# Optimization experiments

Hardware: AMD Instinct MI355X
Metric: run time of the kernel (lower is better)

Reference implementation:

```python
import jax, jax.numpy as jnp
import numpy as np

N, P, K, H, W = 16, 2048, 512, 256, 256
ZTHRESH = 2.0          # PRUN_ZSCORE_THRESHOLD
MULT = 5               # HV_HYPOTHESIS_IN_MASK_MULTIPLIER


def setup_inputs() -> dict:
    key = jax.random.key(0)
    uv_img = jax.random.normal(key, (N, 2, H, W), dtype=jnp.float32)
    rng = np.random.default_rng(0)
    # mask points per instance (torch.where(mask[i]) made fixed-shape)
    pts = rng.integers(0, H, size=(N, P, 2)).astype(np.int32)
    # multinomial pair sampling without replacement: distinct indices per pair
    i0 = rng.integers(0, P, size=(N, K))
    off = rng.integers(1, P, size=(N, K))
    i1 = (i0 + off) % P
    pair_idx = np.stack([i0, i1], axis=-1).astype(np.int32)
    return {"uv_img": uv_img, "pts": jnp.asarray(pts), "pair_idx": jnp.asarray(pair_idx)}


def _gather_uv(uv_img, coords):
    # uv_img: [N,2,H,W], coords: [N,M,2] int -> [N,M,2] uv values
    n, _, h, w = uv_img.shape
    flat = coords[..., 0] * w + coords[..., 1]            # [N,M]
    uv_flat = uv_img.reshape(n, 2, h * w)                 # [N,2,HW]
    g = jnp.take_along_axis(uv_flat, flat[:, None, :], axis=2)  # [N,2,M]
    return jnp.transpose(g, (0, 2, 1))                    # [N,M,2]


def reference(uv_img, pts, pair_idx):
    # --- generate hypotheses (batched pinverse solver) ---
    p0 = jnp.take_along_axis(pts, pair_idx[..., 0:1], axis=1)  # [N,K,2]
    p1 = jnp.take_along_axis(pts, pair_idx[..., 1:2], axis=1)  # [N,K,2]
    uv0 = _gather_uv(uv_img, p0)                               # [N,K,2]
    uv1 = _gather_uv(uv_img, p1)                               # [N,K,2]
    A = jnp.stack((uv0, -uv1), axis=-1)                        # [N,K,2,2]
    Bv = (p1 - p0).astype(jnp.float32)[..., None]              # [N,K,2,1]  (-p0 + p1)
    X = jnp.matmul(jnp.linalg.pinv(A), Bv)                     # [N,K,2,1]
    x0 = X[:, :, 0, :]                                         # [N,K,1]
    Y = x0 * uv0 + p0.astype(jnp.float32)                      # [N,K,2] hypotheses

    # --- prune outliers (z-score, drop -> nan in torch; here masked) ---
    mean = jnp.mean(Y, axis=1, keepdims=True)
    std = jnp.std(Y, axis=1, keepdims=True, ddof=1)
    z = jnp.abs((Y - mean) / std)
    bad = jnp.any(z > ZTHRESH, axis=-1) | jnp.any(jnp.isnan(Y), axis=-1)  # [N,K]
    Yz = jnp.where(bad[..., None], 0.0, Y)                     # nan-hypotheses zeroed (as torch does)

    # --- hypothesis weights ---
    ptsf = pts.astype(jnp.float32)                             # [N,P,2]
    uv_p = _gather_uv(uv_img, pts)                             # [N,P,2]
    d = Y[:, :, None, :] - ptsf[:, None, :, :]                 # [N,K,P,2]
    a = d / jnp.linalg.norm(d, axis=-1, keepdims=True)
    b = jnp.einsum('nkpc,npc->nkp', a, uv_p) > 0               # direction agreement
    w = jnp.sum(b, axis=-1)                                    # [N,K] int
    match = Y.astype(jnp.int32)[:, :, None, :] == pts[:, None, :, :]
    h_in_mask = jnp.sum(match[..., 0] & match[..., 1], axis=-1)  # [N,K]
    factor = jnp.where(h_in_mask == 1, MULT, 1)
    w = (factor * w).astype(jnp.float32)
    w = jnp.where(bad, 0.0, w)                                 # outlier rows get 0 weight
    w = w / jnp.maximum(jnp.sum(w, axis=1, keepdims=True), 1.0)

    weighted_mean = jnp.sum(Yz * w[..., None], axis=1)         # [N,2]
    pixel_xy = weighted_mean[:, ::-1]                          # (row,col) -> (x,y)
    return pixel_xy
```

## Files before the change

kernel.cpp:

```cpp
#include <hip/hip_runtime.h>
#include <math.h>

#define N_ 16
#define P_ 2048
#define K_ 512
#define H_ 256
#define W_ 256
#define HW_ (H_ * W_)
#define ZT_ 2.0f
#define GBLK_ 128
#define KB_ 32
#define KPB_ 16

__global__ __launch_bounds__(256) void k_pre(
    const float* __restrict__ uv_img, const int* __restrict__ pts,
    const int* __restrict__ pair, float2* __restrict__ uvp,
    float2* __restrict__ Yg, int* __restrict__ bad, int* __restrict__ done) {
  int tid = threadIdx.x;
  if (blockIdx.x < GBLK_) {
    int id = blockIdx.x * 256 + tid;
    int2 c = ((const int2*)pts)[id];
    const float* base = uv_img + (size_t)(id >> 11) * 2 * HW_;
    int o = c.x * W_ + c.y;
    uvp[id] = make_float2(base[o], base[HW_ + o]);
    return;
  }
  int n = blockIdx.x - GBLK_;
  if (tid == 0) done[n] = 0;
  const int2* pts2 = (const int2*)pts + n * P_;
  const int2* pr2 = (const int2*)pair + n * K_;
  const float* base = uv_img + (size_t)n * 2 * HW_;

  float2 ya, yb;
#pragma unroll
  for (int h = 0; h < 2; h++) {
    int k = tid + h * 256;
    int2 pr = pr2[k];
    int2 p0 = pts2[pr.x];
    int2 p1 = pts2[pr.y];
    float u00 = base[p0.x * W_ + p0.y];
    float u01 = base[HW_ + p0.x * W_ + p0.y];
    float u10 = base[p1.x * W_ + p1.y];
    float u11 = base[HW_ + p1.x * W_ + p1.y];
    float B0 = (float)(p1.x - p0.x);
    float B1 = (float)(p1.y - p0.y);
    float det = u10 * u01 - u00 * u11;
    float x0 = (u10 * B1 - B0 * u11) / det;
    float2 y = make_float2(x0 * u00 + (float)p0.x, x0 * u01 + (float)p0.y);
    if (h == 0) ya = y; else yb = y;
    Yg[n * K_ + k] = y;
  }

  __shared__ float red[4][2];
  __shared__ float bc[4];
  int wave = tid >> 6, lane = tid & 63;
  float a0 = ya.x + yb.x, a1 = ya.y + yb.y;
  for (int off = 32; off >= 1; off >>= 1) {
    a0 += __shfl_down(a0, off);
    a1 += __shfl_down(a1, off);
  }
  if (lane == 0) { red[wave][0] = a0; red[wave][1] = a1; }
  __syncthreads();
  if (tid == 0) {
    float t0 = red[0][0] + red[1][0] + red[2][0] + red[3][0];
    float t1 = red[0][1] + red[1][1] + red[2][1] + red[3][1];
    bc[0] = t0 / (float)K_;
    bc[1] = t1 / (float)K_;
  }
  __syncthreads();
  float m0 = bc[0], m1 = bc[1];
  float ea0 = ya.x - m0, ea1 = ya.y - m1;
  float eb0 = yb.x - m0, eb1 = yb.y - m1;
  a0 = ea0 * ea0 + eb0 * eb0;
  a1 = ea1 * ea1 + eb1 * eb1;
  for (int off = 32; off >= 1; off >>= 1) {
    a0 += __shfl_down(a0, off);
    a1 += __shfl_down(a1, off);
  }
  if (lane == 0) { red[wave][0] = a0; red[wave][1] = a1; }
  __syncthreads();
  if (tid == 0) {
    float t0 = red[0][0] + red[1][0] + red[2][0] + red[3][0];
    float t1 = red[0][1] + red[1][1] + red[2][1] + red[3][1];
    bc[2] = sqrtf(t0 / (float)(K_ - 1));
    bc[3] = sqrtf(t1 / (float)(K_ - 1));
  }
  __syncthreads();
  float sd0 = bc[2], sd1 = bc[3];
  int bda = (fabsf(ea0 / sd0) > ZT_) | (fabsf(ea1 / sd1) > ZT_) |
            (ya.x != ya.x) | (ya.y != ya.y);
  int bdb = (fabsf(eb0 / sd0) > ZT_) | (fabsf(eb1 / sd1) > ZT_) |
            (yb.x != yb.x) | (yb.y != yb.y);
  bad[n * K_ + tid] = bda;
  bad[n * K_ + tid + 256] = bdb;
}

__global__ __launch_bounds__(256) void k_vote(
    const int* __restrict__ pts, const float2* __restrict__ uvp,
    const float2* __restrict__ Yg, const int* __restrict__ bad,
    float* __restrict__ pw, float* __restrict__ ps0, float* __restrict__ ps1,
    int* __restrict__ done, float* __restrict__ out) {
  int b = blockIdx.x, tid = threadIdx.x;
  int n = b >> 5, kt = b & (KB_ - 1);
  __shared__ float4 sf[P_];
  __shared__ float red[4][3];
  __shared__ int sflag;
  const int2* pts2 = (const int2*)pts + n * P_;
  const float2* uvn = uvp + n * P_;

#pragma unroll
  for (int j = 0; j < 8; j++) {
    int p = j * 256 + tid;
    int2 pc = pts2[p];
    float2 uc = uvn[p];
    float c = (float)pc.x * uc.x + (float)pc.y * uc.y;
    int pk = (pc.x << 8) | pc.y;
    sf[p] = make_float4(uc.x, uc.y, c, __int_as_float(pk));
  }

  int k = kt * KPB_ + (tid >> 4);
  int pl = tid & 15;
  float2 yk = Yg[n * K_ + k];
  int iy0 = (int)yk.x, iy1 = (int)yk.y;
  int mk = (((unsigned)iy0 < 256u) & ((unsigned)iy1 < 256u))
               ? ((iy0 << 8) | iy1) : -1;
  __syncthreads();

  int cnt = 0, hm = 0;
#pragma unroll 8
  for (int i = 0; i < P_ / 16; i++) {
    float4 f = sf[pl + (i << 4)];
    float dot = fmaf(yk.x, f.x, fmaf(yk.y, f.y, -f.z));
    cnt += (dot > 0.f) ? 1 : 0;
    hm += (__float_as_int(f.w) == mk) ? 1 : 0;
  }

  for (int off = 8; off >= 1; off >>= 1) {
    cnt += __shfl_down(cnt, off, 16);
    hm += __shfl_down(hm, off, 16);
  }
  float w = 0.f, s0 = 0.f, s1 = 0.f;
  if (pl == 0 && !bad[n * K_ + k]) {
    w = (float)cnt * ((hm == 1) ? 5.0f : 1.0f);
    s0 = w * yk.x;
    s1 = w * yk.y;
  }
  for (int off = 32; off >= 1; off >>= 1) {
    w += __shfl_down(w, off);
    s0 += __shfl_down(s0, off);
    s1 += __shfl_down(s1, off);
  }
  int wave = tid >> 6, lane = tid & 63;
  if (lane == 0) { red[wave][0] = w; red[wave][1] = s0; red[wave][2] = s1; }
  __syncthreads();
  if (tid == 0) {
    float tw = red[0][0] + red[1][0] + red[2][0] + red[3][0];
    float t0 = red[0][1] + red[1][1] + red[2][1] + red[3][1];
    float t1 = red[0][2] + red[1][2] + red[2][2] + red[3][2];
    pw[b] = tw;
    ps0[b] = t0;
    ps1[b] = t1;
    int old = __hip_atomic_fetch_add(&done[n], 1, __ATOMIC_ACQ_REL,
                                     __HIP_MEMORY_SCOPE_AGENT);
    sflag = (old == KB_ - 1);
  }
  __syncthreads();
  if (sflag && tid < KB_) {
    int i = (n << 5) + tid;
    float fw = __hip_atomic_load(&pw[i], __ATOMIC_RELAXED,
                                 __HIP_MEMORY_SCOPE_AGENT);
    float f0 = __hip_atomic_load(&ps0[i], __ATOMIC_RELAXED,
                                 __HIP_MEMORY_SCOPE_AGENT);
    float f1 = __hip_atomic_load(&ps1[i], __ATOMIC_RELAXED,
                                 __HIP_MEMORY_SCOPE_AGENT);
    for (int off = 16; off >= 1; off >>= 1) {
      fw += __shfl_down(fw, off, 32);
      f0 += __shfl_down(f0, off, 32);
      f1 += __shfl_down(f1, off, 32);
    }
    if (tid == 0) {
      float den = fmaxf(fw, 1.0f);
      out[n * 2 + 0] = f1 / den;
      out[n * 2 + 1] = f0 / den;
    }
  }
}

extern "C" void kernel_launch(void* const* d_in, const int* in_sizes, int n_in,
                              void* d_out, int out_size, void* d_ws,
                              size_t ws_size, hipStream_t stream) {
  const float* uv_img = (const float*)d_in[0];
  const int* pts = (const int*)d_in[1];
  const int* pair = (const int*)d_in[2];
  float* out = (float*)d_out;

  float2* uvp = (float2*)d_ws;
  float2* Yg = uvp + N_ * P_;
  int* bad = (int*)(Yg + N_ * K_);
  float* pw = (float*)(bad + N_ * K_);
  float* ps0 = pw + N_ * KB_;
  float* ps1 = ps0 + N_ * KB_;
  int* done = (int*)(ps1 + N_ * KB_);

  hipLaunchKernelGGL(k_pre, dim3(GBLK_ + N_), dim3(256), 0, stream, uv_img,
                     pts, pair, uvp, Yg, bad, done);
  hipLaunchKernelGGL(k_vote, dim3(N_ * KB_), dim3(256), 0, stream, pts, uvp,
                     Yg, bad, pw, ps0, ps1, done, out);
}
```

Measured before the change: 26.46 us.

## Register-tile hypotheses per thread and stream points directly, dropping shared staging

After: 27.35 us. 1.03x slower.

```diff
diff --git a/kernel.cpp b/kernel.cpp
--- a/kernel.cpp
+++ b/kernel.cpp
@@ -102,64 +102,77 @@
     int* __restrict__ done, float* __restrict__ out) {
   int b = blockIdx.x, tid = threadIdx.x;
   int n = b >> 5, kt = b & (KB_ - 1);
-  __shared__ float4 sf[P_];
+  int wave = tid >> 6, lane = tid & 63;
+  __shared__ unsigned redc[4][KPB_];
   __shared__ float red[4][3];
   __shared__ int sflag;
+
+  float ykx[KPB_], yky[KPB_];
+  int mk[KPB_];
+#pragma unroll
+  for (int j = 0; j < KPB_; j++) {
+    float2 y = Yg[n * K_ + kt * KPB_ + j];
+    ykx[j] = y.x;
+    yky[j] = y.y;
+    int iy0 = (int)y.x, iy1 = (int)y.y;
+    mk[j] = (((unsigned)iy0 < 256u) & ((unsigned)iy1 < 256u))
+                ? ((iy0 << 8) | iy1) : -1;
+  }
+
   const int2* pts2 = (const int2*)pts + n * P_;
   const float2* uvn = uvp + n * P_;
-
-#pragma unroll
-  for (int j = 0; j < 8; j++) {
-    int p = j * 256 + tid;
+  unsigned acc[KPB_];
+#pragma unroll
+  for (int j = 0; j < KPB_; j++) acc[j] = 0u;
+
+#pragma unroll
+  for (int i = 0; i < P_ / 256; i++) {
+    int p = i * 256 + tid;
     int2 pc = pts2[p];
     float2 uc = uvn[p];
-    float c = (float)pc.x * uc.x + (float)pc.y * uc.y;
+    float c = fmaf((float)pc.x, uc.x, (float)pc.y * uc.y);
     int pk = (pc.x << 8) | pc.y;
-    sf[p] = make_float4(uc.x, uc.y, c, __int_as_float(pk));
-  }
-
-  int k = kt * KPB_ + (tid >> 4);
-  int pl = tid & 15;
-  float2 yk = Yg[n * K_ + k];
-  int iy0 = (int)yk.x, iy1 = (int)yk.y;
-  int mk = (((unsigned)iy0 < 256u) & ((unsigned)iy1 < 256u))
-               ? ((iy0 << 8) | iy1) : -1;
-  __syncthreads();
-
-  int cnt = 0, hm = 0;
-#pragma unroll 8
-  for (int i = 0; i < P_ / 16; i++) {
-    float4 f = sf[pl + (i << 4)];
-    float dot = fmaf(yk.x, f.x, fmaf(yk.y, f.y, -f.z));
-    cnt += (dot > 0.f) ? 1 : 0;
-    hm += (__float_as_int(f.w) == mk) ? 1 : 0;
-  }
-
-  for (int off = 8; off >= 1; off >>= 1) {
-    cnt += __shfl_down(cnt, off, 16);
-    hm += __shfl_down(hm, off, 16);
-  }
+#pragma unroll
+    for (int j = 0; j < KPB_; j++) {
+      float dot = fmaf(ykx[j], uc.x, fmaf(yky[j], uc.y, -c));
+      acc[j] += (dot > 0.f ? 1u : 0u) + (pk == mk[j] ? 0x10000u : 0u);
+    }
+  }
+
+#pragma unroll
+  for (int j = 0; j < KPB_; j++) {
+    unsigned a = acc[j];
+    for (int off = 32; off >= 1; off >>= 1)
+      a += (unsigned)__shfl_xor((int)a, off);
+    acc[j] = a;
+  }
+  if (lane == 0) {
+#pragma unroll
+    for (int j = 0; j < KPB_; j++) redc[wave][j] = acc[j];
+  }
+  __syncthreads();
+
   float w = 0.f, s0 = 0.f, s1 = 0.f;
-  if (pl == 0 && !bad[n * K_ + k]) {
-    w = (float)cnt * ((hm == 1) ? 5.0f : 1.0f);
-    s0 = w * yk.x;
-    s1 = w * yk.y;
-  }
-  for (int off = 32; off >= 1; off >>= 1) {
-    w += __shfl_down(w, off);
-    s0 += __shfl_down(s0, off);
-    s1 += __shfl_down(s1, off);
-  }
-  int wave = tid >> 6, lane = tid & 63;
-  if (lane == 0) { red[wave][0] = w; red[wave][1] = s0; red[wave][2] = s1; }
-  __syncthreads();
+  if (tid < KPB_) {
+    unsigned t = redc[0][tid] + redc[1][tid] + redc[2][tid] + redc[3][tid];
+    int cnt = (int)(t & 0xFFFFu), hm = (int)(t >> 16);
+    int k = kt * KPB_ + tid;
+    if (!bad[n * K_ + k]) {
+      float2 y = Yg[n * K_ + k];
+      w = (float)cnt * ((hm == 1) ? 5.0f : 1.0f);
+      s0 = w * y.x;
+      s1 = w * y.y;
+    }
+    for (int off = 8; off >= 1; off >>= 1) {
+      w += __shfl_down(w, off, 16);
+      s0 += __shfl_down(s0, off, 16);
+      s1 += __shfl_down(s1, off, 16);
+    }
+  }
   if (tid == 0) {
-    float tw = red[0][0] + red[1][0] + red[2][0] + red[3][0];
-    float t0 = red[0][1] + red[1][1] + red[2][1] + red[3][1];
-    float t1 = red[0][2] + red[1][2] + red[2][2] + red[3][2];
-    pw[b] = tw;
-    ps0[b] = t0;
-    ps1[b] = t1;
+    pw[b] = w;
+    ps0[b] = s0;
+    ps1[b] = s1;
     int old = __hip_atomic_fetch_add(&done[n], 1, __ATOMIC_ACQ_REL,
                                      __HIP_MEMORY_SCOPE_AGENT);
     sflag = (old == KB_ - 1);
```
